# Kernel tuning notes

Measured on AMD Instinct MI355X. Metric: run time of the kernel, lower is better.

Reference implementation:

```python
import jax, jax.numpy as jnp
import numpy as np
from jax.scipy.special import gammaln

T, G, M = 730, 2000, 4
NEARZERO = 1e-5
UH_LEN = 15

PHY_NAMES = ['inf_pc','inf_hbv_beta','inf_vic_bexp','inf_hmets_alpha','sr_soil_depth_1',
 'bf1_gr4j_x3','bf1_pl_bfc','bf1_pl_bfn','bf1_vic_bfmax','bf1_vic_bfn','bf1_top_bfmax',
 'bf1_top_bfn','bf1_top_lam','bf1_thresh_bfmax','bf1_thresh_bfn','bf1_thresh_bfthresh',
 'perc_gawser_maxperc','crise_hbv_crise','bf2_con_bfmax','bf2_gr4j_x3','bf2_lin_bfc',
 'bf2_pl_bfc','bf2_pl_bfn','bf2_vic_bfmax','bf2_vic_bfn',
 'ddf','Tbm','Tbf','cfr','swi','vadose_max_level']
PHY_BOUNDS = np.array([[0.,1.],[0.5,3.],[0.001,3.],[0.3,1.],[0.05,0.5],
 [20.,300.],[0.001,0.5],[1.,5.],[0.1,50.],[1.,5.],[0.1,50.],
 [1.,5.],[5.,10.],[0.1,50.],[1.,5.],[0.,1.],
 [1.,50.],[0.1,50.],[0.1,50.],[20.,300.],[0.0001,0.1],
 [0.0001,0.1],[1.,5.],[0.1,50.],[1.,5.],
 [0.,20.],[-2.,3.],[-5.,2.],[0.,1.],[0.05,0.4],[10.,500.]], dtype=np.float32)
ROUT_BOUNDS = np.array([[0.3,20.],[0.01,5.],[0.5,13.],[0.15,1.5]], dtype=np.float32)


def uh_gamma(a, theta, L):
    # gamma-distribution unit hydrograph, a/theta: [G] -> [G, L]
    aa = jax.nn.relu(a) + 0.1
    th = jax.nn.relu(theta) + 0.5
    t = jnp.arange(0.5, float(L))  # [L]
    logw = (aa[:, None] - 1.0) * jnp.log(t)[None, :] - t[None, :] / th[:, None] \
           - gammaln(aa)[:, None] - aa[:, None] * jnp.log(th[:, None])
    w = jnp.exp(logw)
    return w / jnp.sum(w, axis=1, keepdims=True)


def route(q, uh):
    # causal per-basin convolution: q [T,G], uh [G,L] -> [T,G]
    L = uh.shape[1]
    x = q.T[None]                 # [1, G, T]
    k = uh[:, None, ::-1]         # [G, 1, L]  (reversed -> true convolution)
    out = jax.lax.conv_general_dilated(x, k, window_strides=(1,),
                                       padding=[(L - 1, 0)],
                                       feature_group_count=G,
                                       dimension_numbers=('NCW', 'OIW', 'NCW'))
    return out[0].T


def _model(x_phy, weights_params, hybrid_params):
    P = len(PHY_NAMES)
    lb = jnp.asarray(PHY_BOUNDS[:, 0]); ub = jnp.asarray(PHY_BOUNDS[:, 1])
    phy = jax.nn.sigmoid(hybrid_params[:, :P * M].reshape(G, P, M))
    phy = lb[None, :, None] + phy * (ub - lb)[None, :, None]       # [G,P,M]
    pd = {n: phy[:, i, :] for i, n in enumerate(PHY_NAMES)}
    rb = jnp.asarray(ROUT_BOUNDS)
    rout = jax.nn.sigmoid(hybrid_params[:, P * M:P * M + 4])
    rout = rb[:, 0][None] + rout * (rb[:, 1] - rb[:, 0])[None]      # [G,4]
    a1, b1, a2, b2 = rout[:, 0], rout[:, 1], rout[:, 2], rout[:, 3]
    # 9 blend weights, softmax within the 3 groups of 3
    w = jax.nn.softmax(weights_params.reshape(T, G, 3, 3, M), axis=3)
    vmax = pd['vadose_max_level']                                   # [G,M]

    def step(carry, xs):
        snow, liqw, cum, vad, phr = carry
        prcp, temp, pet, wt = xs           # [G],[G],[G],[G,3,3,M]
        p = prcp[:, None]; tt = temp[:, None]; pe = pet[:, None]    # [G,M]
        rain = p * (tt >= 0.0)
        snowf = p * (tt < 0.0)
        # --- snow module: 3 parallel snowpacks (HMETS/HBV/VIC style) ---
        t3 = tt[..., None]
        snow = snow + snowf[..., None]
        ddf = pd['ddf'][..., None]
        one = jnp.ones_like(cum[..., 0])
        fac = jnp.stack([one, one, jnp.minimum(1.0 + cum[..., 2] / 100.0, 2.0)], axis=-1)
        melt = jnp.minimum(ddf * fac * jax.nn.relu(t3 - pd['Tbm'][..., None]), snow)
        refr = jnp.minimum(pd['cfr'][..., None] * ddf * jax.nn.relu(pd['Tbf'][..., None] - t3), liqw)
        snow = snow - melt + refr
        liqw = liqw + melt - refr
        cap = pd['swi'][..., None] * snow
        release = jax.nn.relu(liqw - cap)
        liqw = jnp.minimum(liqw, cap)
        cum = jnp.where(snow > 10.0 * NEARZERO, cum + melt, 0.0)
        water = rain + jnp.mean(release, axis=-1)                    # [G,M]
        # --- infiltration: blend of HMETS / HBV / VIC (weights group 1) ---
        sm = jnp.clip(vad / vmax, 1e-4, 1.0 - 1e-4)
        i1 = pd['inf_hmets_alpha'] * water * (1.0 - sm)
        i2 = water * (1.0 - sm ** pd['inf_hbv_beta'])
        i3 = water * (1.0 - sm) ** pd['inf_vic_bexp']
        w1 = wt[:, 0]
        infil = w1[:, 0] * i1 + w1[:, 1] * i2 + w1[:, 2] * i3
        runoff = jax.nn.relu(water - infil)
        # --- baseflow 1 from vadose zone (weights group 2) ---
        q1 = vad * (1.0 - (1.0 + (vad / pd['bf1_gr4j_x3']) ** 4) ** (-0.25))
        q2 = pd['bf1_pl_bfc'] * vmax * sm ** pd['bf1_pl_bfn']
        q3 = pd['bf1_vic_bfmax'] * sm ** pd['bf1_vic_bfn']
        w2 = wt[:, 1]
        bf1 = jnp.minimum(w2[:, 0] * q1 + w2[:, 1] * q2 + w2[:, 2] * q3, vad)
        perc = pd['perc_gawser_maxperc'] * sm
        crise = jnp.minimum(pd['crise_hbv_crise'] * (1.0 - sm), phr)
        aet = pe * sm
        vad_new = vad + infil + crise - bf1 - perc - aet
        over = jax.nn.relu(vad_new - vmax)
        vad = jnp.clip(vad_new, NEARZERO, vmax)
        runoff = runoff + over
        # --- baseflow 2 from phreatic zone (weights group 3) ---
        c1 = jnp.minimum(pd['bf2_con_bfmax'], phr)
        c2 = pd['bf2_lin_bfc'] * phr
        c3 = pd['bf2_vic_bfmax'] * (phr / (phr + pd['bf2_gr4j_x3'])) ** pd['bf2_vic_bfn']
        w3 = wt[:, 2]
        bf2 = jnp.minimum(w3[:, 0] * c1 + w3[:, 1] * c2 + w3[:, 2] * c3, phr)
        phr = jnp.maximum(phr + perc - crise - bf2, NEARZERO)
        outs = (jnp.mean(runoff, -1), jnp.mean(bf1 + bf2, -1),
                jnp.mean(aet, -1), jnp.mean(vad, -1), jnp.mean(phr, -1))
        return (snow, liqw, cum, vad, phr), outs

    s0 = jnp.full((G, M, 3), NEARZERO, dtype=x_phy.dtype)
    carry0 = (s0, s0, s0, 0.5 * vmax, jnp.full((G, M), NEARZERO, dtype=x_phy.dtype))
    xs = (x_phy[:, :, 0], x_phy[:, :, 1], x_phy[:, :, 2], w)
    _, (qk, qb, aet_s, vad_s, phr_s) = jax.lax.scan(step, carry0, xs)
    uh1 = uh_gamma(a1, b1, UH_LEN)
    uh2 = uh_gamma(a2, b2, UH_LEN)
    Q = route(qk, uh1) + route(qb, uh2)   # [T,G]
    return Q, aet_s, vad_s, phr_s


def setup_inputs() -> dict:
    key = jax.random.key(0)
    k1, k2, k3, k4, k5 = jax.random.split(key, 5)
    prcp = jax.nn.relu(jax.random.normal(k1, (T, G)) * 5.0)
    temp = jax.random.normal(k2, (T, G)) * 8.0 + 2.0
    pet = jax.random.uniform(k3, (T, G)) * 5.0
    x_phy = jnp.stack([prcp, temp, pet], axis=-1).astype(jnp.float32)
    weights_params = jax.random.normal(k4, (T, G, 9 * M), dtype=jnp.float32)
    hybrid_params = jax.random.normal(k5, (G, len(PHY_NAMES) * M + 4), dtype=jnp.float32)
    return {'x_phy': x_phy, 'weights_params': weights_params, 'hybrid_params': hybrid_params}


def reference(x_phy, weights_params, hybrid_params):
    return _model(x_phy, weights_params, hybrid_params)
```

## Files before the change

### kernel.cpp

```cpp
#include <hip/hip_runtime.h>


#define TS 730
#define GC 2000
#define MM 4
#define TG (TS*GC)
#define PD 5

__device__ __forceinline__ float fexp(float x){ return __expf(x); }
__device__ __forceinline__ float flog(float x){ return __logf(x); }
__device__ __forceinline__ float frcp(float x){ return __builtin_amdgcn_rcpf(x); }

__device__ __forceinline__ float qsum(float x){
    float y = __int_as_float(__builtin_amdgcn_mov_dpp(__float_as_int(x), 0xB1, 0xF, 0xF, true));
    x += y;
    y = __int_as_float(__builtin_amdgcn_mov_dpp(__float_as_int(x), 0x4E, 0xF, 0xF, true));
    return x + y;
}

__global__ __launch_bounds__(64, 1) void scan_kernel(
    const float* __restrict__ x_phy,
    const float* __restrict__ wts,
    const float* __restrict__ hyb,
    float* __restrict__ out,
    float* __restrict__ qk,
    float* __restrict__ qb)
{
    const int tid = blockIdx.x*64 + threadIdx.x;
    const int g = tid >> 2, m = tid & 3;

    const float* hp = hyb + g*128 + m;
    #define PARAM(i, lo, hi) ((lo) + ((hi)-(lo)) / (1.0f + __expf(-hp[(i)*4])))
    const float beta    = PARAM(1,  0.5f,   3.0f);
    const float bexp    = PARAM(2,  0.001f, 3.0f);
    const float alpha   = PARAM(3,  0.3f,   1.0f);
    const float x3      = PARAM(5,  20.0f,  300.0f);
    const float plbfc   = PARAM(6,  0.001f, 0.5f);
    const float plbfn   = PARAM(7,  1.0f,   5.0f);
    const float vbmax   = PARAM(8,  0.1f,   50.0f);
    const float vbfn    = PARAM(9,  1.0f,   5.0f);
    const float maxperc = PARAM(16, 1.0f,   50.0f);
    const float crise_p = PARAM(17, 0.1f,   50.0f);
    const float c_bfmax = PARAM(18, 0.1f,   50.0f);
    const float g4x3    = PARAM(19, 20.0f,  300.0f);
    const float linbfc  = PARAM(20, 1e-4f,  0.1f);
    const float b2vmax  = PARAM(23, 0.1f,   50.0f);
    const float b2vn    = PARAM(24, 1.0f,   5.0f);
    const float ddf     = PARAM(25, 0.0f,   20.0f);
    const float Tbm     = PARAM(26, -2.0f,  3.0f);
    const float Tbf     = PARAM(27, -5.0f,  2.0f);
    const float cfr     = PARAM(28, 0.0f,   1.0f);
    const float swi     = PARAM(29, 0.05f,  0.4f);
    const float vmax    = PARAM(30, 10.0f,  500.0f);
    #undef PARAM

    const float inv_vmax = 1.0f / vmax;
    const float inv_x3   = 1.0f / x3;
    const float cfr_ddf  = cfr * ddf;
    const float q2c      = plbfc * vmax;

    float snow0 = 1e-5f, snow1 = 1e-5f, snow2 = 1e-5f;
    float liqw0 = 1e-5f, liqw1 = 1e-5f, liqw2 = 1e-5f;
    float cum0  = 1e-5f, cum1  = 1e-5f, cum2  = 1e-5f;
    float vad = 0.5f * vmax;
    float phr = 1e-5f;

    float fp[PD], ft[PD], fe[PD], w_[PD][9];
    #define LOAD_SLOT(k, tn) { \
        const float* xn = x_phy + (tn)*(GC*3)  + g*3; \
        const float* wn = wts   + (tn)*(GC*36) + g*36 + m; \
        fp[k]=xn[0]; ft[k]=xn[1]; fe[k]=xn[2]; \
        w_[k][0]=wn[0];  w_[k][1]=wn[4];  w_[k][2]=wn[8]; \
        w_[k][3]=wn[12]; w_[k][4]=wn[16]; w_[k][5]=wn[20]; \
        w_[k][6]=wn[24]; w_[k][7]=wn[28]; w_[k][8]=wn[32]; }

    #pragma unroll
    for (int k = 0; k < PD; ++k) LOAD_SLOT(k, k);

    for (int tb = 0; tb < TS; tb += PD) {
        #pragma unroll
        for (int k = 0; k < PD; ++k) {
            const int t = tb + k;

            const float p  = fp[k], tt = ft[k], pe = fe[k];
            const float r0 = w_[k][0], r1 = w_[k][1], r2 = w_[k][2];
            const float r3 = w_[k][3], r4 = w_[k][4], r5 = w_[k][5];
            const float r6 = w_[k][6], r7 = w_[k][7], r8 = w_[k][8];
            int tn = t + PD; if (tn >= TS) tn = TS - 1;
            LOAD_SLOT(k, tn);

            const float e0=fexp(r0), e1=fexp(r1), e2=fexp(r2);
            const float e3=fexp(r3), e4=fexp(r4), e5=fexp(r5);
            const float e6=fexp(r6), e7=fexp(r7), e8=fexp(r8);
            const float is1 = frcp(e0+e1+e2);
            const float is2 = frcp(e3+e4+e5);
            const float is3 = frcp(e6+e7+e8);

            const float rain  = (tt >= 0.0f) ? p : 0.0f;
            const float snowf = (tt <  0.0f) ? p : 0.0f;
            const float meltb = ddf     * fmaxf(tt - Tbm, 0.0f);
            const float refrb = cfr_ddf * fmaxf(Tbf - tt, 0.0f);
            const float fac2  = fminf(1.0f + cum2*0.01f, 2.0f);

            float rel0, rel1, rel2;
            {
                snow0 += snowf;
                const float melt = fminf(meltb, snow0);
                const float refr = fminf(refrb, liqw0);
                snow0 = snow0 - melt + refr;
                liqw0 = liqw0 + melt - refr;
                const float cap = swi*snow0;
                rel0 = fmaxf(liqw0 - cap, 0.0f);
                liqw0 = fminf(liqw0, cap);
                cum0 = (snow0 > 1e-4f) ? cum0 + melt : 0.0f;
            }
            {
                snow1 += snowf;
                const float melt = fminf(meltb, snow1);
                const float refr = fminf(refrb, liqw1);
                snow1 = snow1 - melt + refr;
                liqw1 = liqw1 + melt - refr;
                const float cap = swi*snow1;
                rel1 = fmaxf(liqw1 - cap, 0.0f);
                liqw1 = fminf(liqw1, cap);
                cum1 = (snow1 > 1e-4f) ? cum1 + melt : 0.0f;
            }
            {
                snow2 += snowf;
                const float melt = fminf(meltb*fac2, snow2);
                const float refr = fminf(refrb, liqw2);
                snow2 = snow2 - melt + refr;
                liqw2 = liqw2 + melt - refr;
                const float cap = swi*snow2;
                rel2 = fmaxf(liqw2 - cap, 0.0f);
                liqw2 = fminf(liqw2, cap);
                cum2 = (snow2 > 1e-4f) ? cum2 + melt : 0.0f;
            }

            const float water = rain + (rel0+rel1+rel2)*(1.0f/3.0f);

            const float sm     = fminf(fmaxf(vad*inv_vmax, 1e-4f), 1.0f - 1e-4f);
            const float one_sm = 1.0f - sm;
            const float lsm    = flog(sm);
            const float l1sm   = flog(one_sm);
            const float i1 = alpha * water * one_sm;
            const float i2 = water * (1.0f - fexp(beta*lsm));
            const float i3 = water * fexp(bexp*l1sm);
            const float infil = (e0*i1 + e1*i2 + e2*i3) * is1;
            float runoff = fmaxf(water - infil, 0.0f);

            const float y   = vad * inv_x3;
            const float y2  = y*y;
            const float b14 = 1.0f + y2*y2;
            const float q1  = vad * (1.0f - rsqrtf(sqrtf(b14)));
            const float q2  = q2c   * fexp(plbfn*lsm);
            const float q3  = vbmax * fexp(vbfn*lsm);
            const float bf1 = fminf((e3*q1 + e4*q2 + e5*q3) * is2, vad);

            const float perc  = maxperc * sm;
            const float crise = fminf(crise_p * one_sm, phr);
            const float aet   = pe * sm;
            const float vad_new = vad + infil + crise - bf1 - perc - aet;
            const float over  = fmaxf(vad_new - vmax, 0.0f);
            vad = fminf(fmaxf(vad_new, 1e-5f), vmax);
            runoff += over;

            const float c1 = fminf(c_bfmax, phr);
            const float c2 = linbfc * phr;
            const float fr = phr * frcp(phr + g4x3);
            const float c3 = b2vmax * fexp(b2vn * flog(fr));
            const float bf2 = fminf((e6*c1 + e7*c2 + e8*c3) * is3, phr);
            phr = fmaxf(phr + perc - crise - bf2, 1e-5f);

            const float s_run = qsum(runoff);
            const float s_qb  = qsum(bf1 + bf2);
            const float s_aet = qsum(aet);
            const float s_vad = qsum(vad);
            const float s_phr = qsum(phr);
            if (m == 0) {
                const int o = t*GC + g;
                qk[o]         = s_run*0.25f;
                qb[o]         = s_qb *0.25f;
                out[TG   + o] = s_aet*0.25f;
                out[2*TG + o] = s_vad*0.25f;
                out[3*TG + o] = s_phr*0.25f;
            }
        }
    }
    #undef LOAD_SLOT
}

__global__ __launch_bounds__(64) void uh_kernel(
    const float* __restrict__ hyb, float* __restrict__ uh1, float* __restrict__ uh2)
{
    const int g = blockIdx.x*64 + threadIdx.x;
    if (g >= GC) return;
    const float* hp = hyb + g*128 + 124;
    const float s0 = 1.0f/(1.0f + __expf(-hp[0]));
    const float s1 = 1.0f/(1.0f + __expf(-hp[1]));
    const float s2 = 1.0f/(1.0f + __expf(-hp[2]));
    const float s3 = 1.0f/(1.0f + __expf(-hp[3]));
    const float a1 = 0.3f  + (20.0f-0.3f) *s0;
    const float b1 = 0.01f + (5.0f-0.01f) *s1;
    const float a2 = 0.5f  + (13.0f-0.5f) *s2;
    const float b2 = 0.15f + (1.5f-0.15f) *s3;

    #pragma unroll
    for (int which = 0; which < 2; ++which) {
        const float a  = which ? a2 : a1;
        const float th = which ? b2 : b1;
        float* dst = which ? uh2 : uh1;
        const float aa = fmaxf(a, 0.0f) + 0.1f;
        const float tv_inv = 1.0f / (fmaxf(th, 0.0f) + 0.5f);
        float lw[15]; float mx = -1e30f;
        #pragma unroll
        for (int l = 0; l < 15; ++l) {
            const float tv = (float)l + 0.5f;
            lw[l] = (aa - 1.0f)*__logf(tv) - tv*tv_inv;
            mx = fmaxf(mx, lw[l]);
        }
        float w[15]; float s = 0.0f;
        #pragma unroll
        for (int l = 0; l < 15; ++l) { w[l] = __expf(lw[l]-mx); s += w[l]; }
        const float inv_s = 1.0f/s;
        #pragma unroll
        for (int l = 0; l < 15; ++l) dst[l*GC + g] = w[l]*inv_s;
    }
}

__global__ __launch_bounds__(256) void route_kernel(
    const float* __restrict__ qk, const float* __restrict__ qb,
    const float* __restrict__ uh1, const float* __restrict__ uh2,
    float* __restrict__ Q)
{
    const int tid = blockIdx.x*256 + threadIdx.x;
    if (tid >= TG) return;
    const int t = tid / GC;
    const int g = tid - t*GC;
    float acc = 0.0f;
    if (t >= 14) {
        #pragma unroll
        for (int l = 0; l < 15; ++l) {
            const int o = tid - l*GC;
            acc += qk[o]*uh1[l*GC+g] + qb[o]*uh2[l*GC+g];
        }
    } else {
        for (int l = 0; l <= t; ++l) {
            const int o = tid - l*GC;
            acc += qk[o]*uh1[l*GC+g] + qb[o]*uh2[l*GC+g];
        }
    }
    Q[tid] = acc;
}

extern "C" void kernel_launch(void* const* d_in, const int* in_sizes, int n_in,
                              void* d_out, int out_size, void* d_ws, size_t ws_size,
                              hipStream_t stream)
{
    const float* x_phy = (const float*)d_in[0];
    const float* wts   = (const float*)d_in[1];
    const float* hyb   = (const float*)d_in[2];
    float* out = (float*)d_out;
    float* ws  = (float*)d_ws;
    float* qk  = ws;
    float* qb  = ws + TG;
    float* uh1 = ws + 2*TG;
    float* uh2 = ws + 2*TG + 15*GC;

    uh_kernel   <<<(GC+63)/64,   64,  0, stream>>>(hyb, uh1, uh2);
    scan_kernel <<<(GC*MM)/64,   64,  0, stream>>>(x_phy, wts, hyb, out, qk, qb);
    route_kernel<<<(TG+255)/256, 256, 0, stream>>>(qk, qb, uh1, uh2, out);
}
```

Measured before the change: 665.2 us.

## Split per-step mixture terms across 16 lanes and fuse routing into scan

Each basin now uses 16 lanes, one per (member, mixture-term) pair, instead of 4. The three 3-way softmax mixtures are evaluated in parallel with DPP reductions, which shortens the serial per-step dependency chain and quadruples the number of waves in the latency-bound scan. The routing convolution is fused into the scan through a lane-shifted delay line of runoff and baseflow, so the separate route kernel and the qk/qb intermediate buffers go away. In exchange every lane recomputes the snow state, and each timestep adds more cross-lane shuffles.

After: 659.7 us. No clear change (-0.8%).

```diff
diff --git a/kernel.cpp b/kernel.cpp
--- a/kernel.cpp
+++ b/kernel.cpp
@@ -3,31 +3,42 @@
 
 #define TS 730
 #define GC 2000
-#define MM 4
 #define TG (TS*GC)
 #define PD 5
-
-__device__ __forceinline__ float fexp(float x){ return __expf(x); }
-__device__ __forceinline__ float flog(float x){ return __logf(x); }
-__device__ __forceinline__ float frcp(float x){ return __builtin_amdgcn_rcpf(x); }
+#define LOG2E 1.4426950408889634f
+
+__device__ __forceinline__ float frcp (float x){ return __builtin_amdgcn_rcpf(x); }
+__device__ __forceinline__ float fexp2(float x){ return __builtin_amdgcn_exp2f(x); }
+__device__ __forceinline__ float flog2(float x){ return __builtin_amdgcn_logf(x); }
 
 __device__ __forceinline__ float qsum(float x){
-    float y = __int_as_float(__builtin_amdgcn_mov_dpp(__float_as_int(x), 0xB1, 0xF, 0xF, true));
-    x += y;
-    y = __int_as_float(__builtin_amdgcn_mov_dpp(__float_as_int(x), 0x4E, 0xF, 0xF, true));
-    return x + y;
+    x += __int_as_float(__builtin_amdgcn_mov_dpp(__float_as_int(x),0xB1,0xF,0xF,true));
+    x += __int_as_float(__builtin_amdgcn_mov_dpp(__float_as_int(x),0x4E,0xF,0xF,true));
+    return x;
+}
+__device__ __forceinline__ float rshr1(float x){
+    return __int_as_float(__builtin_amdgcn_mov_dpp(__float_as_int(x),0x111,0xF,0xF,true));
+}
+__device__ __forceinline__ float sum16(float x){
+    x = qsum(x);
+    x += __shfl_xor(x, 4, 64);
+    x += __shfl_xor(x, 8, 64);
+    return x;
 }
 
 __global__ __launch_bounds__(64, 1) void scan_kernel(
     const float* __restrict__ x_phy,
     const float* __restrict__ wts,
     const float* __restrict__ hyb,
-    float* __restrict__ out,
-    float* __restrict__ qk,
-    float* __restrict__ qb)
+    const float* __restrict__ uh1,
+    const float* __restrict__ uh2,
+    float* __restrict__ out)
 {
     const int tid = blockIdx.x*64 + threadIdx.x;
-    const int g = tid >> 2, m = tid & 3;
+    const int g  = tid >> 4;
+    const int jj = tid & 15;
+    const int m  = jj >> 2;
+    const int q  = jj & 3;
 
     const float* hp = hyb + g*128 + m;
     #define PARAM(i, lo, hi) ((lo) + ((hi)-(lo)) / (1.0f + __expf(-hp[(i)*4])))
@@ -59,132 +70,120 @@
     const float cfr_ddf  = cfr * ddf;
     const float q2c      = plbfc * vmax;
 
-    float snow0 = 1e-5f, snow1 = 1e-5f, snow2 = 1e-5f;
-    float liqw0 = 1e-5f, liqw1 = 1e-5f, liqw2 = 1e-5f;
-    float cum0  = 1e-5f, cum1  = 1e-5f, cum2  = 1e-5f;
+    #define SELQ(a,b,c,d) ((q==0)?(a):((q==1)?(b):((q==2)?(c):(d))))
+    const float A1  = SELQ(0.0f,  1.0f, 0.0f, 0.0f);
+    const float B1  = SELQ(alpha,-1.0f, 1.0f, 0.0f);
+    const float C1  = SELQ(1.0f,  beta, bexp, 1.0f);
+    const float B2c = SELQ(0.0f,  q2c,  vbmax, 0.0f);
+    const float C2  = SELQ(-0.25f,plbfn,vbfn,  1.0f);
+    const float C3  = SELQ(1.0f,  1.0f, b2vn,  b2vn);
+    const float B3  = SELQ(0.0f,  0.0f, b2vmax,0.0f);
+    const float relw = SELQ(2.0f/3.0f, 1.0f/3.0f, 0.0f, 0.0f);
+    const float ffac = SELQ(0.0f, 0.01f, 0.01f, 0.01f);
+    const float emask = (q==3) ? -16384.0f : 0.0f;
+    const int   qsel  = (q==3) ? 2 : q;
+    #undef SELQ
+
+    float tap1 = 0.0f, tap2 = 0.0f;
+    if (jj < 15) { tap1 = uh1[jj*GC+g]; tap2 = uh2[jj*GC+g]; }
+    float Dk = 0.0f, Db = 0.0f;
+
+    float snow = 1e-5f, liqw = 1e-5f, cum = 1e-5f;
     float vad = 0.5f * vmax;
     float phr = 1e-5f;
 
-    float fp[PD], ft[PD], fe[PD], w_[PD][9];
+    float fp[PD], ft[PD], fe[PD], wa[PD], wb[PD], wc[PD];
     #define LOAD_SLOT(k, tn) { \
         const float* xn = x_phy + (tn)*(GC*3)  + g*3; \
-        const float* wn = wts   + (tn)*(GC*36) + g*36 + m; \
+        const float* wn = wts   + (tn)*(GC*36) + g*36 + qsel*4 + m; \
         fp[k]=xn[0]; ft[k]=xn[1]; fe[k]=xn[2]; \
-        w_[k][0]=wn[0];  w_[k][1]=wn[4];  w_[k][2]=wn[8]; \
-        w_[k][3]=wn[12]; w_[k][4]=wn[16]; w_[k][5]=wn[20]; \
-        w_[k][6]=wn[24]; w_[k][7]=wn[28]; w_[k][8]=wn[32]; }
+        wa[k]=wn[0]; wb[k]=wn[12]; wc[k]=wn[24]; }
 
     #pragma unroll
     for (int k = 0; k < PD; ++k) LOAD_SLOT(k, k);
 
+    int o = g;
     for (int tb = 0; tb < TS; tb += PD) {
         #pragma unroll
         for (int k = 0; k < PD; ++k) {
             const int t = tb + k;
-
             const float p  = fp[k], tt = ft[k], pe = fe[k];
-            const float r0 = w_[k][0], r1 = w_[k][1], r2 = w_[k][2];
-            const float r3 = w_[k][3], r4 = w_[k][4], r5 = w_[k][5];
-            const float r6 = w_[k][6], r7 = w_[k][7], r8 = w_[k][8];
+            const float r0 = wa[k], r1 = wb[k], r2 = wc[k];
             int tn = t + PD; if (tn >= TS) tn = TS - 1;
             LOAD_SLOT(k, tn);
 
-            const float e0=fexp(r0), e1=fexp(r1), e2=fexp(r2);
-            const float e3=fexp(r3), e4=fexp(r4), e5=fexp(r5);
-            const float e6=fexp(r6), e7=fexp(r7), e8=fexp(r8);
-            const float is1 = frcp(e0+e1+e2);
-            const float is2 = frcp(e3+e4+e5);
-            const float is3 = frcp(e6+e7+e8);
+            const float e0 = fexp2(fmaf(r0, LOG2E, emask));
+            const float e1 = fexp2(fmaf(r1, LOG2E, emask));
+            const float e2 = fexp2(fmaf(r2, LOG2E, emask));
+            const float is1 = frcp(qsum(e0));
+            const float is2 = frcp(qsum(e1));
+            const float is3 = frcp(qsum(e2));
+
+            const float fr = phr * frcp(phr + g4x3);
+            const float E3 = fexp2(C3 * flog2(fr));
+            const float cv = (q==0) ? fminf(c_bfmax, phr)
+                           : ((q==1) ? linbfc*phr : B3*E3);
+            const float bf2 = fminf(qsum(e2*cv)*is3, phr);
 
             const float rain  = (tt >= 0.0f) ? p : 0.0f;
             const float snowf = (tt <  0.0f) ? p : 0.0f;
             const float meltb = ddf     * fmaxf(tt - Tbm, 0.0f);
             const float refrb = cfr_ddf * fmaxf(Tbf - tt, 0.0f);
-            const float fac2  = fminf(1.0f + cum2*0.01f, 2.0f);
-
-            float rel0, rel1, rel2;
-            {
-                snow0 += snowf;
-                const float melt = fminf(meltb, snow0);
-                const float refr = fminf(refrb, liqw0);
-                snow0 = snow0 - melt + refr;
-                liqw0 = liqw0 + melt - refr;
-                const float cap = swi*snow0;
-                rel0 = fmaxf(liqw0 - cap, 0.0f);
-                liqw0 = fminf(liqw0, cap);
-                cum0 = (snow0 > 1e-4f) ? cum0 + melt : 0.0f;
+            const float fac   = fminf(fmaf(cum, ffac, 1.0f), 2.0f);
+            snow += snowf;
+            const float melt = fminf(meltb*fac, snow);
+            const float refr = fminf(refrb, liqw);
+            snow = snow - melt + refr;
+            liqw = liqw + melt - refr;
+            const float cap = swi*snow;
+            const float rel = fmaxf(liqw - cap, 0.0f);
+            liqw = fminf(liqw, cap);
+            cum = (snow > 1e-4f) ? cum + melt : 0.0f;
+            const float water = rain + qsum(rel*relw);
+
+            const float sm     = fminf(fmaxf(vad*inv_vmax, 1e-4f), 1.0f-1e-4f);
+            const float one_sm = 1.0f - sm;
+            const float S1 = (q==1) ? sm : one_sm;
+            const float E1 = fexp2(C1 * flog2(S1));
+            const float iv = water * fmaf(B1, E1, A1);
+            const float infil = qsum(e0*iv) * is1;
+
+            const float y  = vad*inv_x3;
+            const float y2 = y*y;
+            const float S2 = (q==0) ? fmaf(y2, y2, 1.0f) : sm;
+            const float E2 = fexp2(C2 * flog2(S2));
+            const float A2 = (q==0) ?  vad : 0.0f;
+            const float B2 = (q==0) ? -vad : B2c;
+            const float qv = fmaf(B2, E2, A2);
+            const float bf1 = fminf(qsum(e1*qv)*is2, vad);
+
+            float runoff = fmaxf(water - infil, 0.0f);
+            const float perc  = maxperc*sm;
+            const float crise = fminf(crise_p*one_sm, phr);
+            const float aet   = pe*sm;
+            const float vad_new = vad + infil + crise - bf1 - perc - aet;
+            runoff += fmaxf(vad_new - vmax, 0.0f);
+            vad = fminf(fmaxf(vad_new, 1e-5f), vmax);
+            phr = fmaxf(phr + perc - crise - bf2, 1e-5f);
+
+            const float s_run = sum16(runoff)   * 0.0625f;
+            const float s_qb  = sum16(bf1+bf2)  * 0.0625f;
+            const float s_aet = sum16(aet)      * 0.0625f;
+            const float s_vad = sum16(vad)      * 0.0625f;
+            const float s_phr = sum16(phr)      * 0.0625f;
+
+            const float shk = rshr1(Dk), shb = rshr1(Db);
+            Dk = (jj==0) ? s_run : shk;
+            Db = (jj==0) ? s_qb  : shb;
+            const float Q = sum16(fmaf(Dk, tap1, Db*tap2));
+
+            if (jj == 0) {
+                out[o]        = Q;
+                out[TG   + o] = s_aet;
+                out[2*TG + o] = s_vad;
+                out[3*TG + o] = s_phr;
             }
-            {
-                snow1 += snowf;
-                const float melt = fminf(meltb, snow1);
-                const float refr = fminf(refrb, liqw1);
-                snow1 = snow1 - melt + refr;
-                liqw1 = liqw1 + melt - refr;
-                const float cap = swi*snow1;
-                rel1 = fmaxf(liqw1 - cap, 0.0f);
-                liqw1 = fminf(liqw1, cap);
-                cum1 = (snow1 > 1e-4f) ? cum1 + melt : 0.0f;
-            }
-            {
-                snow2 += snowf;
-                const float melt = fminf(meltb*fac2, snow2);
-                const float refr = fminf(refrb, liqw2);
-                snow2 = snow2 - melt + refr;
-                liqw2 = liqw2 + melt - refr;
-                const float cap = swi*snow2;
-                rel2 = fmaxf(liqw2 - cap, 0.0f);
-                liqw2 = fminf(liqw2, cap);
-                cum2 = (snow2 > 1e-4f) ? cum2 + melt : 0.0f;
-            }
-
-            const float water = rain + (rel0+rel1+rel2)*(1.0f/3.0f);
-
-            const float sm     = fminf(fmaxf(vad*inv_vmax, 1e-4f), 1.0f - 1e-4f);
-            const float one_sm = 1.0f - sm;
-            const float lsm    = flog(sm);
-            const float l1sm   = flog(one_sm);
-            const float i1 = alpha * water * one_sm;
-            const float i2 = water * (1.0f - fexp(beta*lsm));
-            const float i3 = water * fexp(bexp*l1sm);
-            const float infil = (e0*i1 + e1*i2 + e2*i3) * is1;
-            float runoff = fmaxf(water - infil, 0.0f);
-
-            const float y   = vad * inv_x3;
-            const float y2  = y*y;
-            const float b14 = 1.0f + y2*y2;
-            const float q1  = vad * (1.0f - rsqrtf(sqrtf(b14)));
-            const float q2  = q2c   * fexp(plbfn*lsm);
-            const float q3  = vbmax * fexp(vbfn*lsm);
-            const float bf1 = fminf((e3*q1 + e4*q2 + e5*q3) * is2, vad);
-
-            const float perc  = maxperc * sm;
-            const float crise = fminf(crise_p * one_sm, phr);
-            const float aet   = pe * sm;
-            const float vad_new = vad + infil + crise - bf1 - perc - aet;
-            const float over  = fmaxf(vad_new - vmax, 0.0f);
-            vad = fminf(fmaxf(vad_new, 1e-5f), vmax);
-            runoff += over;
-
-            const float c1 = fminf(c_bfmax, phr);
-            const float c2 = linbfc * phr;
-            const float fr = phr * frcp(phr + g4x3);
-            const float c3 = b2vmax * fexp(b2vn * flog(fr));
-            const float bf2 = fminf((e6*c1 + e7*c2 + e8*c3) * is3, phr);
-            phr = fmaxf(phr + perc - crise - bf2, 1e-5f);
-
-            const float s_run = qsum(runoff);
-            const float s_qb  = qsum(bf1 + bf2);
-            const float s_aet = qsum(aet);
-            const float s_vad = qsum(vad);
-            const float s_phr = qsum(phr);
-            if (m == 0) {
-                const int o = t*GC + g;
-                qk[o]         = s_run*0.25f;
-                qb[o]         = s_qb *0.25f;
-                out[TG   + o] = s_aet*0.25f;
-                out[2*TG + o] = s_vad*0.25f;
-                out[3*TG + o] = s_phr*0.25f;
-            }
+            o += GC;
         }
     }
     #undef LOAD_SLOT
@@ -228,31 +227,6 @@
     }
 }
 
-__global__ __launch_bounds__(256) void route_kernel(
-    const float* __restrict__ qk, const float* __restrict__ qb,
-    const float* __restrict__ uh1, const float* __restrict__ uh2,
-    float* __restrict__ Q)
-{
-    const int tid = blockIdx.x*256 + threadIdx.x;
-    if (tid >= TG) return;
-    const int t = tid / GC;
-    const int g = tid - t*GC;
-    float acc = 0.0f;
-    if (t >= 14) {
-        #pragma unroll
-        for (int l = 0; l < 15; ++l) {
-            const int o = tid - l*GC;
-            acc += qk[o]*uh1[l*GC+g] + qb[o]*uh2[l*GC+g];
-        }
-    } else {
-        for (int l = 0; l <= t; ++l) {
-            const int o = tid - l*GC;
-            acc += qk[o]*uh1[l*GC+g] + qb[o]*uh2[l*GC+g];
-        }
-    }
-    Q[tid] = acc;
-}
-
 extern "C" void kernel_launch(void* const* d_in, const int* in_sizes, int n_in,
                               void* d_out, int out_size, void* d_ws, size_t ws_size,
                               hipStream_t stream)
@@ -262,12 +236,9 @@
     const float* hyb   = (const float*)d_in[2];
     float* out = (float*)d_out;
     float* ws  = (float*)d_ws;
-    float* qk  = ws;
-    float* qb  = ws + TG;
-    float* uh1 = ws + 2*TG;
-    float* uh2 = ws + 2*TG + 15*GC;
-
-    uh_kernel   <<<(GC+63)/64,   64,  0, stream>>>(hyb, uh1, uh2);
-    scan_kernel <<<(GC*MM)/64,   64,  0, stream>>>(x_phy, wts, hyb, out, qk, qb);
-    route_kernel<<<(TG+255)/256, 256, 0, stream>>>(qk, qb, uh1, uh2, out);
-}
+    float* uh1 = ws;
+    float* uh2 = ws + 15*GC;
+
+    uh_kernel  <<<(GC+63)/64, 64, 0, stream>>>(hyb, uh1, uh2);
+    scan_kernel<<<GC*16/64,   64, 0, stream>>>(x_phy, wts, hyb, uh1, uh2, out);
+}
```
